# Kernel tuning notes

Hardware: AMD Instinct MI355X
Metric: run time of the kernel (lower is better)

The kernel has to match this reference:

```python
import jax, jax.numpy as jnp
import numpy as np

MAXDISP = 192  # must match init_kwargs max_disp


def _interp_axis(x, axis, out_size):
    """1-D linear interpolation along `axis` with align_corners=True."""
    in_size = x.shape[axis]
    src = jnp.arange(out_size, dtype=jnp.float32) * ((in_size - 1) / (out_size - 1))
    i0 = jnp.clip(jnp.floor(src).astype(jnp.int32), 0, in_size - 1)
    i1 = jnp.clip(i0 + 1, 0, in_size - 1)
    w = (src - i0.astype(jnp.float32)).astype(x.dtype)
    shape = [1] * x.ndim
    shape[axis] = out_size
    w = w.reshape(shape)
    return jnp.take(x, i0, axis=axis) * (1 - w) + jnp.take(x, i1, axis=axis) * w


def create_cost_volume(left, right, maxdisp):
    """Vectorized version of the original per-disparity slice-copy loop.
    cost[:, :C, d, :, w] = left[:, :, :, w]        if w >= d else 0
    cost[:, C:, d, :, w] = right[:, :, :, w - d]   if w >= d else 0
    Returns [B, 2C, D, H, W] with D = maxdisp // 4.
    """
    B, C, H, W = left.shape
    D = maxdisp // 4
    d = jnp.arange(D)[:, None]          # [D,1]
    w = jnp.arange(W)[None, :]          # [1,W]
    mask = (w >= d).astype(left.dtype)  # [D,W]
    idx = jnp.clip(w - d, 0, W - 1)     # [D,W] shifted gather indices
    mask_b = mask[None, None, :, None, :]                       # [1,1,D,1,W]
    cost_left = left[:, :, None, :, :] * mask_b                 # [B,C,D,H,W]
    cost_right = jnp.take(right, idx.reshape(-1), axis=3)       # [B,C,H,D*W]
    cost_right = cost_right.reshape(B, C, H, D, W)
    cost_right = jnp.transpose(cost_right, (0, 1, 3, 2, 4)) * mask_b
    return jnp.concatenate([cost_left, cost_right], axis=1)     # [B,2C,D,H,W]


def upsample_regression(vol, maxdisp):
    """Trilinear x4 upsample (align_corners=True) + softmax over disparity +
    soft-argmin expectation. vol: [B, D/4, H/4, W/4] -> [B, H, W]."""
    x = vol
    for axis in (1, 2, 3):
        x = _interp_axis(x, axis, x.shape[axis] * 4)
    p = jax.nn.softmax(x, axis=1)                       # [B, maxdisp, H, W]
    disps = jnp.arange(maxdisp, dtype=x.dtype)
    return jnp.einsum('bdhw,d->bhw', p, disps)


def setup_inputs() -> dict:
    key = jax.random.key(0)
    k1, k2 = jax.random.split(key)
    left = jax.random.normal(k1, (2, 32, 64, 128), dtype=jnp.float32)
    right = jax.random.normal(k2, (2, 32, 64, 128), dtype=jnp.float32)
    return {"left": left, "right": right}


def reference(left, right):
    cost = create_cost_volume(left, right, MAXDISP)  # [B,2C,D,H,W]
    # Stand-in for the (unavailable) stacked hourglass 3D-CNN: channel mean
    # reduces the cost volume to a single-channel disparity volume [B,D,H,W].
    vol = cost.mean(axis=1)
    return upsample_regression(vol, MAXDISP)  # [B, 4H, 4W]
```

## Files before the change

### kernel.cpp

```cpp
#include <hip/hip_runtime.h>

#define BB 2
#define CC 32
#define HC 64
#define WC 128
#define DC 48
#define HO 256
#define WO 512
#define MAXD 192

__global__ __launch_bounds__(256) void sum_channels_kernel(
    const float* __restrict__ left, const float* __restrict__ right,
    float* __restrict__ Ls, float* __restrict__ Rs) {
    __shared__ float sbuf[2][WC];
    int blk = blockIdx.x;
    int m   = blk >> 7;
    int b   = (blk >> 6) & 1;
    int h   = blk & (HC - 1);
    int t   = threadIdx.x;
    int sel = t >> 7;
    int w   = t & (WC - 1);

    const float* src = (m ? right : left)
                     + (size_t)b * (CC * HC * WC)
                     + (size_t)(sel * 16) * (HC * WC) + h * WC + w;
    float s = 0.f;
#pragma unroll
    for (int c = 0; c < 16; ++c) s += src[c * (HC * WC)];
    sbuf[sel][w] = s;
    __syncthreads();
    if (t < WC) {
        float* dst = m ? Rs : Ls;
        dst[b * (HC * WC) + h * WC + t] = sbuf[0][t] + sbuf[1][t];
    }
}

template <int K>
__device__ inline void quarter_work(const float* __restrict__ Rh,
                                    int w0, int w1, float c0, float c1,
                                    float lw0, float lw1,
                                    float& plsum, float& pssum) {
    constexpr int DDLO = 48 * K;
    constexpr int DDHI = 48 * K + 47;
    constexpr int DLO  = (DDLO * (DC - 1)) / (MAXD - 1);
    constexpr int DHI  = (DDHI * (DC - 1)) / (MAXD - 1);
    constexpr int NV   = DHI - DLO + 2;

    float vv[NV];
#pragma unroll
    for (int j = 0; j < NV; ++j) {
        int d = DLO + j;
        if (d > DC - 1) { vv[j] = vv[j - 1]; continue; }
        int i0 = w0 - d; float m0 = (i0 >= 0) ? 1.f : 0.f; i0 = max(i0, 0);
        int i1 = w1 - d; float m1 = (i1 >= 0) ? 1.f : 0.f; i1 = max(i1, 0);
        vv[j] = m0 * c0 * (lw0 + Rh[i0]) + m1 * c1 * (lw1 + Rh[i1]);
    }
    float ls = 0.f, ss = 0.f;
#pragma unroll
    for (int dd = DDLO; dd <= DDHI; ++dd) {
        int d    = (dd * (DC - 1)) / (MAXD - 1);
        float wd = (float)dd * (47.0f / 191.0f) - (float)d;
        float vc = vv[d - DLO];
        float x  = vc + wd * (vv[d - DLO + 1] - vc);
        float e  = __expf(x);
        ls += e;
        ss += e * (float)dd;
    }
    plsum = ls;
    pssum = ss;
}

__global__ __launch_bounds__(512) void disparity_kernel(
    const float* __restrict__ Ls, const float* __restrict__ Rs,
    float* __restrict__ out) {
    __shared__ float Lh[WC];
    __shared__ float Rh[WC];
    __shared__ float redL[4][WC];
    __shared__ float redS[4][WC];

    int blk = blockIdx.x;
    int r   = blk >> 2;
    int g   = blk & 3;
    int b   = r >> 8;
    int hh  = r & (HO - 1);

    float src_h = (float)hh * (63.0f / 255.0f);
    int h0 = (int)src_h; if (h0 > HC - 1) h0 = HC - 1;
    int h1 = min(h0 + 1, HC - 1);
    float fh = src_h - (float)h0;

    int t = threadIdx.x;

    if (t < WC) {
        const float* p = Ls + b * (HC * WC) + t;
        Lh[t] = (1.f - fh) * p[h0 * WC] + fh * p[h1 * WC];
    } else if (t < 2 * WC) {
        int u = t - WC;
        const float* p = Rs + b * (HC * WC) + u;
        Rh[u] = (1.f - fh) * p[h0 * WC] + fh * p[h1 * WC];
    }
    __syncthreads();

    int p = t & (WC - 1);
    int k = t >> 7;
    int ww = g * WC + p;

    float src_w = (float)ww * (127.0f / 511.0f);
    int w0 = (int)src_w; if (w0 > WC - 1) w0 = WC - 1;
    int w1 = min(w0 + 1, WC - 1);
    float fw = src_w - (float)w0;

    const float scale = 1.0f / 64.0f;
    float c0 = (1.f - fw) * scale;
    float c1 = fw * scale;
    float lw0 = Lh[w0];
    float lw1 = Lh[w1];

    float pls, pss;
    switch (k) {
        case 0: quarter_work<0>(Rh, w0, w1, c0, c1, lw0, lw1, pls, pss); break;
        case 1: quarter_work<1>(Rh, w0, w1, c0, c1, lw0, lw1, pls, pss); break;
        case 2: quarter_work<2>(Rh, w0, w1, c0, c1, lw0, lw1, pls, pss); break;
        default: quarter_work<3>(Rh, w0, w1, c0, c1, lw0, lw1, pls, pss); break;
    }
    redL[k][p] = pls;
    redS[k][p] = pss;
    __syncthreads();

    if (t < WC) {
        float ls = redL[0][t] + redL[1][t] + redL[2][t] + redL[3][t];
        float ss = redS[0][t] + redS[1][t] + redS[2][t] + redS[3][t];
        out[r * WO + g * WC + t] = ss / ls;
    }
}

extern "C" void kernel_launch(void* const* d_in, const int* in_sizes, int n_in,
                              void* d_out, int out_size, void* d_ws, size_t ws_size,
                              hipStream_t stream) {
    const float* left  = (const float*)d_in[0];
    const float* right = (const float*)d_in[1];
    float* out = (float*)d_out;
    float* Ls  = (float*)d_ws;
    float* Rs  = Ls + BB * HC * WC;

    sum_channels_kernel<<<256, 256, 0, stream>>>(left, right, Ls, Rs);
    disparity_kernel<<<BB * HO * 4, 512, 0, stream>>>(Ls, Rs, out);
}
```

Baseline: 70.74 us.

## Split disparity range into eighths and double blocks in both kernels

The channel-sum kernel now splits each row into two halves and sums across 4 channel groups, doubling its grid. The disparity kernel splits the 192 disparities into 8 slices of 24 per thread over 64 output columns, which doubles the block count and shortens each thread's serial exp chain. It also uses two accumulators to break the add dependency and adds a launch-bounds occupancy hint. The costs are a larger shared-memory reduction and more redundant height interpolation per output pixel.

After: 71.18 us. Within noise of the previous version (+0.6%).

```diff
diff --git a/kernel.cpp b/kernel.cpp
--- a/kernel.cpp
+++ b/kernel.cpp
@@ -12,36 +12,38 @@
 __global__ __launch_bounds__(256) void sum_channels_kernel(
     const float* __restrict__ left, const float* __restrict__ right,
     float* __restrict__ Ls, float* __restrict__ Rs) {
-    __shared__ float sbuf[2][WC];
+    __shared__ float sbuf[4][64];
     int blk = blockIdx.x;
-    int m   = blk >> 7;
-    int b   = (blk >> 6) & 1;
-    int h   = blk & (HC - 1);
+    int m   = blk >> 8;
+    int b   = (blk >> 7) & 1;
+    int h   = (blk >> 1) & (HC - 1);
+    int wh  = blk & 1;
     int t   = threadIdx.x;
-    int sel = t >> 7;
-    int w   = t & (WC - 1);
+    int sel = t >> 6;
+    int w   = wh * 64 + (t & 63);
 
     const float* src = (m ? right : left)
                      + (size_t)b * (CC * HC * WC)
-                     + (size_t)(sel * 16) * (HC * WC) + h * WC + w;
+                     + (size_t)(sel * 8) * (HC * WC) + h * WC + w;
     float s = 0.f;
 #pragma unroll
-    for (int c = 0; c < 16; ++c) s += src[c * (HC * WC)];
-    sbuf[sel][w] = s;
+    for (int c = 0; c < 8; ++c) s += src[c * (HC * WC)];
+    sbuf[sel][t & 63] = s;
     __syncthreads();
-    if (t < WC) {
+    if (t < 64) {
         float* dst = m ? Rs : Ls;
-        dst[b * (HC * WC) + h * WC + t] = sbuf[0][t] + sbuf[1][t];
+        dst[b * (HC * WC) + h * WC + wh * 64 + t] =
+            sbuf[0][t] + sbuf[1][t] + sbuf[2][t] + sbuf[3][t];
     }
 }
 
 template <int K>
-__device__ inline void quarter_work(const float* __restrict__ Rh,
-                                    int w0, int w1, float c0, float c1,
-                                    float lw0, float lw1,
-                                    float& plsum, float& pssum) {
-    constexpr int DDLO = 48 * K;
-    constexpr int DDHI = 48 * K + 47;
+__device__ inline void eighth_work(const float* __restrict__ Rh,
+                                   int w0, int w1, float c0, float c1,
+                                   float lw0, float lw1,
+                                   float& plsum, float& pssum) {
+    constexpr int DDLO = 24 * K;
+    constexpr int DDHI = 24 * K + 23;
     constexpr int DLO  = (DDLO * (DC - 1)) / (MAXD - 1);
     constexpr int DHI  = (DDHI * (DC - 1)) / (MAXD - 1);
     constexpr int NV   = DHI - DLO + 2;
@@ -55,7 +57,7 @@
         int i1 = w1 - d; float m1 = (i1 >= 0) ? 1.f : 0.f; i1 = max(i1, 0);
         vv[j] = m0 * c0 * (lw0 + Rh[i0]) + m1 * c1 * (lw1 + Rh[i1]);
     }
-    float ls = 0.f, ss = 0.f;
+    float ls0 = 0.f, ls1 = 0.f, ss0 = 0.f, ss1 = 0.f;
 #pragma unroll
     for (int dd = DDLO; dd <= DDHI; ++dd) {
         int d    = (dd * (DC - 1)) / (MAXD - 1);
@@ -63,24 +65,24 @@
         float vc = vv[d - DLO];
         float x  = vc + wd * (vv[d - DLO + 1] - vc);
         float e  = __expf(x);
-        ls += e;
-        ss += e * (float)dd;
+        if (dd & 1) { ls1 += e; ss1 += e * (float)dd; }
+        else        { ls0 += e; ss0 += e * (float)dd; }
     }
-    plsum = ls;
-    pssum = ss;
+    plsum = ls0 + ls1;
+    pssum = ss0 + ss1;
 }
 
-__global__ __launch_bounds__(512) void disparity_kernel(
+__global__ __launch_bounds__(512, 8) void disparity_kernel(
     const float* __restrict__ Ls, const float* __restrict__ Rs,
     float* __restrict__ out) {
     __shared__ float Lh[WC];
     __shared__ float Rh[WC];
-    __shared__ float redL[4][WC];
-    __shared__ float redS[4][WC];
+    __shared__ float redL[8][64];
+    __shared__ float redS[8][64];
 
     int blk = blockIdx.x;
-    int r   = blk >> 2;
-    int g   = blk & 3;
+    int r   = blk >> 3;
+    int g   = blk & 7;
     int b   = r >> 8;
     int hh  = r & (HO - 1);
 
@@ -101,9 +103,9 @@
     }
     __syncthreads();
 
-    int p = t & (WC - 1);
-    int k = t >> 7;
-    int ww = g * WC + p;
+    int p = t & 63;
+    int k = t >> 6;
+    int ww = g * 64 + p;
 
     float src_w = (float)ww * (127.0f / 511.0f);
     int w0 = (int)src_w; if (w0 > WC - 1) w0 = WC - 1;
@@ -118,19 +120,24 @@
 
     float pls, pss;
     switch (k) {
-        case 0: quarter_work<0>(Rh, w0, w1, c0, c1, lw0, lw1, pls, pss); break;
-        case 1: quarter_work<1>(Rh, w0, w1, c0, c1, lw0, lw1, pls, pss); break;
-        case 2: quarter_work<2>(Rh, w0, w1, c0, c1, lw0, lw1, pls, pss); break;
-        default: quarter_work<3>(Rh, w0, w1, c0, c1, lw0, lw1, pls, pss); break;
+        case 0: eighth_work<0>(Rh, w0, w1, c0, c1, lw0, lw1, pls, pss); break;
+        case 1: eighth_work<1>(Rh, w0, w1, c0, c1, lw0, lw1, pls, pss); break;
+        case 2: eighth_work<2>(Rh, w0, w1, c0, c1, lw0, lw1, pls, pss); break;
+        case 3: eighth_work<3>(Rh, w0, w1, c0, c1, lw0, lw1, pls, pss); break;
+        case 4: eighth_work<4>(Rh, w0, w1, c0, c1, lw0, lw1, pls, pss); break;
+        case 5: eighth_work<5>(Rh, w0, w1, c0, c1, lw0, lw1, pls, pss); break;
+        case 6: eighth_work<6>(Rh, w0, w1, c0, c1, lw0, lw1, pls, pss); break;
+        default: eighth_work<7>(Rh, w0, w1, c0, c1, lw0, lw1, pls, pss); break;
     }
     redL[k][p] = pls;
     redS[k][p] = pss;
     __syncthreads();
 
-    if (t < WC) {
-        float ls = redL[0][t] + redL[1][t] + redL[2][t] + redL[3][t];
-        float ss = redS[0][t] + redS[1][t] + redS[2][t] + redS[3][t];
-        out[r * WO + g * WC + t] = ss / ls;
+    if (t < 64) {
+        float ls = 0.f, ss = 0.f;
+#pragma unroll
+        for (int q = 0; q < 8; ++q) { ls += redL[q][t]; ss += redS[q][t]; }
+        out[r * WO + g * 64 + t] = ss / ls;
     }
 }
 
@@ -143,6 +150,6 @@
     float* Ls  = (float*)d_ws;
     float* Rs  = Ls + BB * HC * WC;
 
-    sum_channels_kernel<<<256, 256, 0, stream>>>(left, right, Ls, Rs);
-    disparity_kernel<<<BB * HO * 4, 512, 0, stream>>>(Ls, Rs, out);
+    sum_channels_kernel<<<512, 256, 0, stream>>>(left, right, Ls, Rs);
+    disparity_kernel<<<BB * HO * 8, 512, 0, stream>>>(Ls, Rs, out);
 }
```

## Fuse channel summation into disparity kernel and split softmax accumulators

Applied to the files above, without the earlier changes.

Removes the separate channel-sum kernel. Each disparity block now sums the 32 channels of left and right directly, for the two source rows it needs, using float4 loads and shared-memory partial sums. This saves a kernel launch and the workspace round trip. In exchange it redundantly re-reads input channel data: 2048 blocks each read about 64KB, versus a single pass before, though most of that should hit in cache. The exp accumulation is also split into even and odd accumulators to shorten dependency chains.

After: 72.66 us. 2.7% more time.

```diff
diff --git a/kernel.cpp b/kernel.cpp
--- a/kernel.cpp
+++ b/kernel.cpp
@@ -8,32 +8,6 @@
 #define HO 256
 #define WO 512
 #define MAXD 192
-
-__global__ __launch_bounds__(256) void sum_channels_kernel(
-    const float* __restrict__ left, const float* __restrict__ right,
-    float* __restrict__ Ls, float* __restrict__ Rs) {
-    __shared__ float sbuf[2][WC];
-    int blk = blockIdx.x;
-    int m   = blk >> 7;
-    int b   = (blk >> 6) & 1;
-    int h   = blk & (HC - 1);
-    int t   = threadIdx.x;
-    int sel = t >> 7;
-    int w   = t & (WC - 1);
-
-    const float* src = (m ? right : left)
-                     + (size_t)b * (CC * HC * WC)
-                     + (size_t)(sel * 16) * (HC * WC) + h * WC + w;
-    float s = 0.f;
-#pragma unroll
-    for (int c = 0; c < 16; ++c) s += src[c * (HC * WC)];
-    sbuf[sel][w] = s;
-    __syncthreads();
-    if (t < WC) {
-        float* dst = m ? Rs : Ls;
-        dst[b * (HC * WC) + h * WC + t] = sbuf[0][t] + sbuf[1][t];
-    }
-}
 
 template <int K>
 __device__ inline void quarter_work(const float* __restrict__ Rh,
@@ -55,7 +29,7 @@
         int i1 = w1 - d; float m1 = (i1 >= 0) ? 1.f : 0.f; i1 = max(i1, 0);
         vv[j] = m0 * c0 * (lw0 + Rh[i0]) + m1 * c1 * (lw1 + Rh[i1]);
     }
-    float ls = 0.f, ss = 0.f;
+    float ls0 = 0.f, ls1 = 0.f, ss0 = 0.f, ss1 = 0.f;
 #pragma unroll
     for (int dd = DDLO; dd <= DDHI; ++dd) {
         int d    = (dd * (DC - 1)) / (MAXD - 1);
@@ -63,16 +37,17 @@
         float vc = vv[d - DLO];
         float x  = vc + wd * (vv[d - DLO + 1] - vc);
         float e  = __expf(x);
-        ls += e;
-        ss += e * (float)dd;
+        if (dd & 1) { ls1 += e; ss1 += e * (float)dd; }
+        else        { ls0 += e; ss0 += e * (float)dd; }
     }
-    plsum = ls;
-    pssum = ss;
+    plsum = ls0 + ls1;
+    pssum = ss0 + ss1;
 }
 
-__global__ __launch_bounds__(512) void disparity_kernel(
-    const float* __restrict__ Ls, const float* __restrict__ Rs,
+__global__ __launch_bounds__(512) void fused_disparity_kernel(
+    const float* __restrict__ left, const float* __restrict__ right,
     float* __restrict__ out) {
+    __shared__ float sbuf[4][4][WC];
     __shared__ float Lh[WC];
     __shared__ float Rh[WC];
     __shared__ float redL[4][WC];
@@ -91,13 +66,34 @@
 
     int t = threadIdx.x;
 
+    {
+        int rsel = t >> 7;
+        int rest = t & (WC - 1);
+        int cq   = rest >> 5;
+        int q    = rest & 31;
+        int hrow = (rsel & 1) ? h1 : h0;
+        const float* src = ((rsel < 2) ? left : right)
+                         + (size_t)b * (CC * HC * WC)
+                         + (size_t)(cq * 8) * (HC * WC) + hrow * WC + q * 4;
+        float4 acc = make_float4(0.f, 0.f, 0.f, 0.f);
+#pragma unroll
+        for (int i = 0; i < 8; ++i) {
+            float4 v = *(const float4*)(src + (size_t)i * (HC * WC));
+            acc.x += v.x; acc.y += v.y; acc.z += v.z; acc.w += v.w;
+        }
+        *(float4*)&sbuf[rsel][cq][q * 4] = acc;
+    }
+    __syncthreads();
+
     if (t < WC) {
-        const float* p = Ls + b * (HC * WC) + t;
-        Lh[t] = (1.f - fh) * p[h0 * WC] + fh * p[h1 * WC];
+        float a0 = sbuf[0][0][t] + sbuf[0][1][t] + sbuf[0][2][t] + sbuf[0][3][t];
+        float a1 = sbuf[1][0][t] + sbuf[1][1][t] + sbuf[1][2][t] + sbuf[1][3][t];
+        Lh[t] = (1.f - fh) * a0 + fh * a1;
     } else if (t < 2 * WC) {
         int u = t - WC;
-        const float* p = Rs + b * (HC * WC) + u;
-        Rh[u] = (1.f - fh) * p[h0 * WC] + fh * p[h1 * WC];
+        float a0 = sbuf[2][0][u] + sbuf[2][1][u] + sbuf[2][2][u] + sbuf[2][3][u];
+        float a1 = sbuf[3][0][u] + sbuf[3][1][u] + sbuf[3][2][u] + sbuf[3][3][u];
+        Rh[u] = (1.f - fh) * a0 + fh * a1;
     }
     __syncthreads();
 
@@ -140,9 +136,7 @@
     const float* left  = (const float*)d_in[0];
     const float* right = (const float*)d_in[1];
     float* out = (float*)d_out;
-    float* Ls  = (float*)d_ws;
-    float* Rs  = Ls + BB * HC * WC;
+    (void)d_ws; (void)ws_size;
 
-    sum_channels_kernel<<<256, 256, 0, stream>>>(left, right, Ls, Rs);
-    disparity_kernel<<<BB * HO * 4, 512, 0, stream>>>(Ls, Rs, out);
+    fused_disparity_kernel<<<BB * HO * 4, 512, 0, stream>>>(left, right, out);
 }
```
